# Optimization experiments

Hardware: AMD Instinct MI355X
Metric: run time of the kernel (lower is better)

Reference implementation:

```python
import jax, jax.numpy as jnp
import numpy as np

D = 128      # input_dim (= out_channels = edge_dim)
H = 2        # n_head
N_ENT = 100000
B = 64       # number of queries / batches
R = 500      # number of relations
E = 400000   # number of original edges
NEG = 0.2    # GATv2 leaky_relu negative slope


def setup_inputs() -> dict:
    key = jax.random.key(0)
    ks = jax.random.split(key, 10)
    s = 1.0 / np.sqrt(D)
    queries = jax.random.normal(ks[0], (B, D), jnp.float32)
    entities = jax.random.normal(ks[1], (N_ENT, D), jnp.float32)
    edge_index = jax.random.randint(ks[2], (2, E), 0, N_ENT)
    relations = jax.random.normal(ks[3], (R, D), jnp.float32)
    relation_index = jax.random.randint(ks[4], (E,), 0, R)
    # guarantees batch.max()+1 == queries.shape[0] (module assert)
    batch = jnp.arange(N_ENT, dtype=jnp.int32) % B
    # GATv2Conv params: lin_l / lin_r (bias=True), lin_edge (bias=False), att, bias
    W_l = jax.random.normal(ks[5], (H * D, D), jnp.float32) * s
    b_l = jnp.zeros((H * D,), jnp.float32)
    W_r = jax.random.normal(ks[6], (H * D, D), jnp.float32) * s
    b_r = jnp.zeros((H * D,), jnp.float32)
    W_ea = jax.random.normal(ks[7], (H * D, D), jnp.float32) * s
    att = jax.random.normal(ks[8], (H, D), jnp.float32) * s
    bias = jnp.zeros((D,), jnp.float32)  # concat=False -> size out_channels
    # outer Injector.lin_edge: Linear(H*D, D, bias=True)
    W_le = jax.random.normal(ks[9], (D, H * D), jnp.float32) / np.sqrt(H * D)
    b_le = jnp.zeros((D,), jnp.float32)
    return dict(queries=queries, entities=entities, edge_index=edge_index,
                relations=relations, relation_index=relation_index, batch=batch,
                W_l=W_l, b_l=b_l, W_r=W_r, b_r=b_r, W_ea=W_ea, att=att,
                bias=bias, W_le=W_le, b_le=b_le)


def reference(queries, entities, edge_index, relations, relation_index, batch,
              W_l, b_l, W_r, b_r, W_ea, att, bias, W_le, b_le):
    n_ent = entities.shape[0]
    node = jnp.vstack([entities, queries])                        # [N+B, D]
    rel_feat = jnp.vstack([relations,
                           jnp.ones((1, relations.shape[1]), relations.dtype)])
    # added edges: query -> its entities
    src = jnp.concatenate([edge_index[0], batch.astype(edge_index.dtype) + n_ent])
    tgt = jnp.concatenate([edge_index[1],
                           jnp.arange(n_ent, dtype=edge_index.dtype)])
    rel_idx = jnp.concatenate([relation_index,
                               jnp.full((n_ent,), rel_feat.shape[0] - 1,
                                        relation_index.dtype)])
    edge_attr = rel_feat[rel_idx]                                  # [Etot, D]

    n_tot = node.shape[0]
    x_l = (node @ W_l.T + b_l).reshape(n_tot, H, D)                # source proj
    x_r = (node @ W_r.T + b_r).reshape(n_tot, H, D)                # target proj
    e = (edge_attr @ W_ea.T).reshape(-1, H, D)                     # [Etot, H, D]

    xj = x_l[src]                                                  # gather per edge
    z = jax.nn.leaky_relu(xj + x_r[tgt] + e, NEG)                  # [Etot, H, D]
    alpha = jnp.einsum('ehd,hd->eh', z, att)                       # [Etot, H]
    # segment softmax over target nodes
    amax = jax.ops.segment_max(alpha, tgt, num_segments=n_tot)
    alpha = jnp.exp(alpha - amax[tgt])
    denom = jax.ops.segment_sum(alpha, tgt, num_segments=n_tot)
    alpha = alpha / (denom[tgt] + 1e-16)

    msg = xj * alpha[..., None]                                    # [Etot, H, D]
    agg = jax.ops.segment_sum(msg, tgt, num_segments=n_tot)        # [Ntot, H, D]
    out = agg.mean(axis=1) + bias                                  # concat=False
    out_node = out[:n_ent]

    out_edge = jax.nn.relu(relations @ W_ea.T)                     # [R, H*D]
    out_edge = out_edge @ W_le.T + b_le                            # [R, D]
    return (out_node, out_edge)
```

## Files before the change

kernel.cpp:

```cpp
#include <hip/hip_runtime.h>
#include <math.h>

#define D 128
#define HD 256
#define N_ENT 100000
#define NBATCH 64
#define NTOT (N_ENT + NBATCH)
#define RCOUNT 500
#define E_BASE 400000
#define ETOT (E_BASE + N_ENT)
#define NEG 0.2f
#define SCAN_NB 391
#define CPAD (SCAN_NB * 256)

#define WCAST_NB 64
#define REL_NB (RCOUNT + 1)
#define PREP_NB (WCAST_NB + REL_NB)

#define GEMM_NB ((NTOT + 63) / 64)
#define HIST_NB ((ETOT + 255) / 256)
#define EDGE_NB 6250

typedef __attribute__((ext_vector_type(8))) short bf16x8;
typedef __attribute__((ext_vector_type(8))) unsigned short u16x8;
typedef __attribute__((ext_vector_type(4))) float f32x4;
typedef __attribute__((ext_vector_type(2))) float f32x2;

static __device__ __forceinline__ unsigned cvt_pk_bf16(float lo, float hi) {
  unsigned r;
  asm("v_cvt_pk_bf16_f32 %0, %1, %2" : "=v"(r) : "v"(lo), "v"(hi));
  return r;
}
static __device__ __forceinline__ unsigned short f2bf_hw(float f) {
  unsigned r;
  asm("v_cvt_pk_bf16_f32 %0, %1, %1" : "=v"(r) : "v"(f));
  return (unsigned short)r;
}
static __device__ __forceinline__ f32x2 bfpair(unsigned u) {
  f32x2 r;
  r[0] = __builtin_bit_cast(float, u << 16);
  r[1] = __builtin_bit_cast(float, u & 0xffff0000u);
  return r;
}

static __device__ __forceinline__ void lds_barrier() {
  __builtin_amdgcn_sched_barrier(0);
  asm volatile("s_waitcnt lgkmcnt(0)" ::: "memory");
  __builtin_amdgcn_sched_barrier(0);
  __builtin_amdgcn_s_barrier();
  __builtin_amdgcn_sched_barrier(0);
}

static __device__ __forceinline__ float dpp_red16(float p) {
  int t;
  t = __builtin_amdgcn_update_dpp(0, __builtin_bit_cast(int, p), 0xB1, 0xF, 0xF, true);
  p += __builtin_bit_cast(float, t);
  t = __builtin_amdgcn_update_dpp(0, __builtin_bit_cast(int, p), 0x4E, 0xF, 0xF, true);
  p += __builtin_bit_cast(float, t);
  t = __builtin_amdgcn_update_dpp(0, __builtin_bit_cast(int, p), 0x141, 0xF, 0xF, true);
  p += __builtin_bit_cast(float, t);
  t = __builtin_amdgcn_update_dpp(0, __builtin_bit_cast(int, p), 0x140, 0xF, 0xF, true);
  p += __builtin_bit_cast(float, t);
  return p;
}

__global__ __launch_bounds__(256) void k_prep(
    const float* __restrict__ W_l, const float* __restrict__ W_r,
    unsigned short* __restrict__ Wbf,
    const float* __restrict__ relations, const float* __restrict__ W_ea,
    const float* __restrict__ W_le, const float* __restrict__ b_le,
    unsigned short* __restrict__ e_rel, float* __restrict__ out_edge) {
  __shared__ float relu_p[HD];
  int bx = blockIdx.x;
  int tid = threadIdx.x;
  if (bx < WCAST_NB) {
    int e4 = (bx * 256 + tid) * 4;
    int v = e4 >> 7;
    int k = e4 & 127;
    const float* src = (v < HD) ? (W_l + (size_t)v * D + k) : (W_r + (size_t)(v - HD) * D + k);
    float4 a = *(const float4*)src;
    uint2 p;
    p.x = cvt_pk_bf16(a.x, a.y);
    p.y = cvt_pk_bf16(a.z, a.w);
    *(uint2*)(Wbf + (size_t)v * D + k) = p;
    return;
  }
  int r = bx - WCAST_NB;
  int j = tid;
  const float* w = W_ea + (size_t)j * D;
  float acc = 0.f;
  if (r < RCOUNT) {
    const float* rel = relations + (size_t)r * D;
    for (int k = 0; k < D; k += 4) {
      float4 a = *(const float4*)(rel + k);
      float4 b = *(const float4*)(w + k);
      acc += a.x * b.x + a.y * b.y + a.z * b.z + a.w * b.w;
    }
  } else {
    for (int k = 0; k < D; k += 4) {
      float4 b = *(const float4*)(w + k);
      acc += b.x + b.y + b.z + b.w;
    }
  }
  e_rel[(size_t)r * HD + j] = f2bf_hw(acc);
  if (r < RCOUNT) {
    relu_p[j] = acc > 0.f ? acc : 0.f;
    __syncthreads();
    if (j < D) {
      const float* wl = W_le + (size_t)j * HD;
      float o = b_le[j];
      for (int k = 0; k < HD; k += 4) {
        float4 p4 = *(const float4*)(relu_p + k);
        float4 w4 = *(const float4*)(wl + k);
        o += p4.x * w4.x + p4.y * w4.y + p4.z * w4.z + p4.w * w4.w;
      }
      out_edge[(size_t)r * D + j] = o;
    }
  }
}

#define LDA 136

__global__ __launch_bounds__(256) void k_gemm_mfma(
    const float* __restrict__ entities, const float* __restrict__ queries,
    const unsigned short* __restrict__ Wbf,
    const float* __restrict__ b_l, const float* __restrict__ b_r,
    unsigned short* __restrict__ x_l, unsigned short* __restrict__ x_r,
    const int* __restrict__ edge_index, const int* __restrict__ relation_index,
    const int* __restrict__ batch, int* __restrict__ counts,
    unsigned* __restrict__ tr, unsigned* __restrict__ key) {
  __shared__ unsigned short AsCs[64 * LDA];
  int tid = threadIdx.x;
  if (blockIdx.x >= GEMM_NB) {
    int e = (blockIdx.x - GEMM_NB) * 256 + tid;
    if (e < ETOT) {
      int s, t, r;
      if (e < E_BASE) {
        s = edge_index[e];
        t = edge_index[E_BASE + e];
        r = relation_index[e];
      } else {
        int i = e - E_BASE;
        s = N_ENT + batch[i];
        t = i;
        r = RCOUNT;
      }
      int rk = atomicAdd(counts + t, 1);
      tr[e] = (unsigned)t | ((unsigned)rk << 17);
      key[e] = (unsigned)s | ((unsigned)r << 17);
    }
    return;
  }
  int rb = blockIdx.x;

  {
    int rr = tid >> 2;
    int part = (tid & 3) * 32;
    int row = rb * 64 + rr;
    const float* sp;
    if (row < N_ENT) sp = entities + (size_t)row * D;
    else if (row < NTOT) sp = queries + (size_t)(row - N_ENT) * D;
    else sp = entities;
#pragma unroll
    for (int k = 0; k < 32; k += 8) {
      float4 a0 = *(const float4*)(sp + part + k);
      float4 a1 = *(const float4*)(sp + part + k + 4);
      uint4 p;
      p.x = cvt_pk_bf16(a0.x, a0.y);
      p.y = cvt_pk_bf16(a0.z, a0.w);
      p.z = cvt_pk_bf16(a1.x, a1.y);
      p.w = cvt_pk_bf16(a1.z, a1.w);
      *(uint4*)(&AsCs[rr * LDA + part + k]) = p;
    }
  }
  __syncthreads();

  int w = tid >> 6, lane = tid & 63;
  int wr = w >> 1, wc = w & 1;
  int m = lane & 15, q8 = (lane >> 4) * 8;

  bf16x8 afr[4][2];
#pragma unroll
  for (int k4 = 0; k4 < 4; k4++)
#pragma unroll
    for (int i = 0; i < 2; i++)
      afr[k4][i] = *(const bf16x8*)(&AsCs[(wr * 32 + i * 16 + m) * LDA + k4 * 32 + q8]);

  for (int ccv = 0; ccv < 4; ccv++) {
    bool isL = ccv < 2;
    const float* bv = isL ? b_l : b_r;
    unsigned short* xdst = isL ? x_l : x_r;
    int cbase = (ccv & 1) * 128;

    f32x4 acc[2][4];
#pragma unroll
    for (int i = 0; i < 2; i++)
#pragma unroll
      for (int j = 0; j < 4; j++) acc[i][j] = (f32x4){0.f, 0.f, 0.f, 0.f};

    const unsigned short* wbase = Wbf + (size_t)(ccv * 128 + wc * 64 + m) * D;
#pragma unroll
    for (int k4 = 0; k4 < 4; k4++) {
      bf16x8 bfr[4];
#pragma unroll
      for (int j = 0; j < 4; j++)
        bfr[j] = *(const bf16x8*)(wbase + (size_t)j * 16 * D + k4 * 32 + q8);
#pragma unroll
      for (int i = 0; i < 2; i++)
#pragma unroll
        for (int j = 0; j < 4; j++)
          acc[i][j] = __builtin_amdgcn_mfma_f32_16x16x32_bf16(afr[k4][i], bfr[j], acc[i][j], 0, 0, 0);
    }

    lds_barrier();
#pragma unroll
    for (int j = 0; j < 4; j++) {
      int col = wc * 64 + j * 16 + m;
      float bb = bv[cbase + col];
#pragma unroll
      for (int i = 0; i < 2; i++) {
        int row0 = wr * 32 + i * 16 + (lane >> 4) * 4;
#pragma unroll
        for (int r = 0; r < 4; r++)
          AsCs[(row0 + r) * LDA + col] = f2bf_hw(acc[i][j][r] + bb);
      }
    }
    lds_barrier();
#pragma unroll
    for (int it = 0; it < 4; it++) {
      int g = it * 256 + tid;
      int row = g >> 4, c8 = (g & 15) * 8;
      int grow = rb * 64 + row;
      if (grow < NTOT) {
        u16x8 v = *(const u16x8*)(&AsCs[row * LDA + c8]);
        *(u16x8*)(xdst + (size_t)grow * HD + cbase + c8) = v;
      }
    }
  }
}

__global__ __launch_bounds__(256) void k_scan_a(const int* __restrict__ counts, int* __restrict__ bsum) {
  __shared__ int sd[256];
  int tid = threadIdx.x;
  sd[tid] = counts[blockIdx.x * 256 + tid];
  __syncthreads();
  for (int off = 128; off > 0; off >>= 1) {
    if (tid < off) sd[tid] += sd[tid + off];
    __syncthreads();
  }
  if (tid == 0) bsum[blockIdx.x] = sd[0];
}

__global__ __launch_bounds__(256) void k_scan_b(
    const int* __restrict__ counts, const int* __restrict__ bsum,
    int* __restrict__ offsets) {
  __shared__ int s[256];
  int b = blockIdx.x, tid = threadIdx.x;
  int part = 0;
  if (tid < b) part += bsum[tid];
  if (tid + 256 < b) part += bsum[tid + 256];
  s[tid] = part;
  __syncthreads();
  for (int off = 128; off > 0; off >>= 1) {
    if (tid < off) s[tid] += s[tid + off];
    __syncthreads();
  }
  int pre_sum = s[0];
  __syncthreads();
  int v = counts[b * 256 + tid];
  s[tid] = v;
  __syncthreads();
  for (int off = 1; off < 256; off <<= 1) {
    int y = (tid >= off) ? s[tid - off] : 0;
    __syncthreads();
    s[tid] += y;
    __syncthreads();
  }
  int excl = pre_sum + s[tid] - v;
  int i = b * 256 + tid;
  if (i <= N_ENT) offsets[i] = excl;
}

__global__ void k_scatter(const unsigned* __restrict__ tr, const unsigned* __restrict__ key,
                          const int* __restrict__ offsets, unsigned* __restrict__ sorted) {
  int e = blockIdx.x * 256 + threadIdx.x;
  if (e >= ETOT) return;
  unsigned a = tr[e];
  sorted[offsets[a & 0x1FFFFu] + (a >> 17)] = key[e];
}

static __device__ __forceinline__ float edge_accum(
    u16x8 xl8, u16x8 er8, const f32x2* __restrict__ xr2,
    const f32x2* __restrict__ at2, f32x2* __restrict__ x2) {
  uint4 xu = __builtin_bit_cast(uint4, xl8);
  uint4 eu = __builtin_bit_cast(uint4, er8);
  unsigned xw[4] = {xu.x, xu.y, xu.z, xu.w};
  unsigned ew[4] = {eu.x, eu.y, eu.z, eu.w};
  f32x2 p2 = (f32x2){0.f, 0.f};
#pragma unroll
  for (int i = 0; i < 4; ++i) {
    f32x2 x = bfpair(xw[i]);
    x2[i] = x;
    f32x2 z = (x + xr2[i]) + bfpair(ew[i]);
    f32x2 zn = z * NEG;
    z[0] = fmaxf(z[0], zn[0]);
    z[1] = fmaxf(z[1], zn[1]);
    p2 += z * at2[i];
  }
  return p2[0] + p2[1];
}

__global__ __launch_bounds__(256) void k_edge(
    const unsigned short* __restrict__ x_l, const unsigned short* __restrict__ x_r,
    const unsigned short* __restrict__ e_rel, const int* __restrict__ offsets,
    const unsigned* __restrict__ sorted, const float* __restrict__ att,
    const float* __restrict__ bias, float* __restrict__ out) {
  int wv = threadIdx.x >> 6;
  int lane = threadIdx.x & 63;
  int half = lane >> 5;
  int sl = lane & 31;
  int elem = sl * 8;
  int t0 = (blockIdx.x * 4 + wv) * 4;

  const char* xlb = (const char*)x_l + elem * 2;
  const char* erb = (const char*)e_rel + elem * 2;

  f32x2 at2[4];
  {
    float4 a0 = *(const float4*)(att + elem);
    float4 a1 = *(const float4*)(att + elem + 4);
    at2[0] = (f32x2){a0.x, a0.y};
    at2[1] = (f32x2){a0.z, a0.w};
    at2[2] = (f32x2){a1.x, a1.y};
    at2[3] = (f32x2){a1.z, a1.w};
  }
  int4 ofs = *(const int4*)(offsets + t0);
  int eb[5];
  eb[0] = ofs.x; eb[1] = ofs.y; eb[2] = ofs.z; eb[3] = ofs.w;
  eb[4] = offsets[t0 + 4];

  u16x8 xr8 = __builtin_nontemporal_load((const u16x8*)(x_r + (size_t)t0 * HD + elem));

#pragma unroll
  for (int ti = 0; ti < 4; ++ti) {
    f32x2 xr2[4];
    {
      uint4 u = __builtin_bit_cast(uint4, xr8);
      xr2[0] = bfpair(u.x); xr2[1] = bfpair(u.y);
      xr2[2] = bfpair(u.z); xr2[3] = bfpair(u.w);
    }
    xr8 = __builtin_nontemporal_load((const u16x8*)(x_r + (size_t)(t0 + ti + 1) * HD + elem));

    int e0 = eb[ti], e1 = eb[ti + 1];
    f32x2 acc2[4];
    acc2[0] = acc2[1] = acc2[2] = acc2[3] = (f32x2){0.f, 0.f};
    float denom = 0.f;
    int e = e0;
    for (; e + 4 <= e1; e += 4) {
      unsigned srA = sorted[e + half];
      unsigned srB = sorted[e + 2 + half];
      u16x8 xlA = *(const u16x8*)(xlb + ((size_t)(srA & 0x1FFFFu) << 9));
      u16x8 erA = *(const u16x8*)(erb + ((size_t)(srA >> 17) << 9));
      u16x8 xlB = *(const u16x8*)(xlb + ((size_t)(srB & 0x1FFFFu) << 9));
      u16x8 erB = *(const u16x8*)(erb + ((size_t)(srB >> 17) << 9));
      f32x2 xa2[4], xb2[4];
      float pa = edge_accum(xlA, erA, xr2, at2, xa2);
      float pb = edge_accum(xlB, erB, xr2, at2, xb2);
      pa = dpp_red16(pa);
      pb = dpp_red16(pb);
      float wa = __expf(pa);
      float wb = __expf(pb);
      denom += wa + wb;
#pragma unroll
      for (int i = 0; i < 4; ++i) {
        acc2[i] += xa2[i] * wa;
        acc2[i] += xb2[i] * wb;
      }
    }
    for (; e < e1; e += 2) {
      int ee = e + half;
      bool valid = ee < e1;
      unsigned sr = sorted[valid ? ee : e0];
      u16x8 xl8 = *(const u16x8*)(xlb + ((size_t)(sr & 0x1FFFFu) << 9));
      u16x8 er8 = *(const u16x8*)(erb + ((size_t)(sr >> 17) << 9));
      f32x2 x2[4];
      float p = edge_accum(xl8, er8, xr2, at2, x2);
      p = dpp_red16(p);
      float wgt = valid ? __expf(p) : 0.f;
      denom += wgt;
#pragma unroll
      for (int i = 0; i < 4; ++i) acc2[i] += x2[i] * wgt;
    }
    denom += __shfl_xor(denom, 32, 64);
#pragma unroll
    for (int i = 0; i < 4; ++i) {
      acc2[i][0] += __shfl_xor(acc2[i][0], 32, 64);
      acc2[i][1] += __shfl_xor(acc2[i][1], 32, 64);
    }
    float inv = 0.5f / (denom + 1e-16f);
    float o[8];
#pragma unroll
    for (int i = 0; i < 4; ++i) {
      o[2 * i] = acc2[i][0] * inv;
      o[2 * i + 1] = acc2[i][1] * inv;
    }
#pragma unroll
    for (int i = 0; i < 8; ++i) o[i] += __shfl_xor(o[i], 16, 64);
    if (lane < 16) {
      int t = t0 + ti;
      int d = sl * 8;
      float4 b0 = *(const float4*)(bias + d);
      float4 b1 = *(const float4*)(bias + d + 4);
      f32x4 s0 = (f32x4){o[0] + b0.x, o[1] + b0.y, o[2] + b0.z, o[3] + b0.w};
      f32x4 s1 = (f32x4){o[4] + b1.x, o[5] + b1.y, o[6] + b1.z, o[7] + b1.w};
      __builtin_nontemporal_store(s0, (f32x4*)(out + (size_t)t * D + d));
      __builtin_nontemporal_store(s1, (f32x4*)(out + (size_t)t * D + d + 4));
    }
  }
}

extern "C" void kernel_launch(void* const* d_in, const int* in_sizes, int n_in,
                              void* d_out, int out_size, void* d_ws, size_t ws_size,
                              hipStream_t stream) {
  const float* queries = (const float*)d_in[0];
  const float* entities = (const float*)d_in[1];
  const int* edge_index = (const int*)d_in[2];
  const float* relations = (const float*)d_in[3];
  const int* relation_index = (const int*)d_in[4];
  const int* batch = (const int*)d_in[5];
  const float* W_l = (const float*)d_in[6];
  const float* b_l = (const float*)d_in[7];
  const float* W_r = (const float*)d_in[8];
  const float* b_r = (const float*)d_in[9];
  const float* W_ea = (const float*)d_in[10];
  const float* att = (const float*)d_in[11];
  const float* bias = (const float*)d_in[12];
  const float* W_le = (const float*)d_in[13];
  const float* b_le = (const float*)d_in[14];

  float* out_node = (float*)d_out;
  float* out_edge = out_node + (size_t)N_ENT * D;

  char* base = (char*)d_ws;
  size_t off = 0;
  auto take = [&](size_t nbytes) -> void* {
    void* p = base + off;
    off += (nbytes + 255) & ~(size_t)255;
    return p;
  };
  unsigned short* x_l = (unsigned short*)take((size_t)NTOT * HD * sizeof(unsigned short));
  unsigned short* x_r = (unsigned short*)take((size_t)NTOT * HD * sizeof(unsigned short));
  unsigned short* e_rel = (unsigned short*)take((size_t)(RCOUNT + 1) * HD * sizeof(unsigned short));
  unsigned short* Wbf = (unsigned short*)take((size_t)512 * D * sizeof(unsigned short));
  int* counts = (int*)take((size_t)CPAD * sizeof(int));
  int* offsets = (int*)take((size_t)(N_ENT + 1) * sizeof(int));
  unsigned* tr = (unsigned*)take((size_t)ETOT * sizeof(unsigned));
  unsigned* key = (unsigned*)take((size_t)ETOT * sizeof(unsigned));
  int* bsum = (int*)take(512 * sizeof(int));
  unsigned* sorted = (unsigned*)take((size_t)ETOT * sizeof(unsigned));

  hipMemsetAsync(counts, 0, (size_t)CPAD * sizeof(int), stream);
  k_prep<<<dim3(PREP_NB), dim3(256), 0, stream>>>(W_l, W_r, Wbf, relations, W_ea, W_le, b_le,
                                                  e_rel, out_edge);
  k_gemm_mfma<<<dim3(GEMM_NB + HIST_NB), dim3(256), 0, stream>>>(entities, queries, Wbf, b_l, b_r,
                                                                 x_l, x_r, edge_index, relation_index,
                                                                 batch, counts, tr, key);
  k_scan_a<<<dim3(SCAN_NB), dim3(256), 0, stream>>>(counts, bsum);
  k_scan_b<<<dim3(SCAN_NB), dim3(256), 0, stream>>>(counts, bsum, offsets);
  k_scatter<<<dim3(HIST_NB), dim3(256), 0, stream>>>(tr, key, offsets, sorted);
  k_edge<<<dim3(EDGE_NB), dim3(256), 0, stream>>>(x_l, x_r, e_rel, offsets, sorted, att, bias, out_node);
}
```

Before: 285.9 us.

## Fold relation prep into GEMM launch and compute block sums via atomics

Moves the relation projection and out_edge computation from the prep kernel into extra blocks of the GEMM/histogram kernel, leaving prep to only cast weights. The histogram blocks now also atomically accumulate per-256-node block sums, which removes the separate scan_a reduction kernel. The bsum array is placed after counts so one memset clears both. This cuts two launches and a pass over counts, at the cost of an extra global atomic per edge on a small, heavily contended array.

Result: slower. 509.0 us (+78.0%).

```diff
diff --git a/kernel.cpp b/kernel.cpp
--- a/kernel.cpp
+++ b/kernel.cpp
@@ -15,7 +15,6 @@
 
 #define WCAST_NB 64
 #define REL_NB (RCOUNT + 1)
-#define PREP_NB (WCAST_NB + REL_NB)
 
 #define GEMM_NB ((NTOT + 63) / 64)
 #define HIST_NB ((ETOT + 255) / 256)
@@ -66,57 +65,16 @@
 
 __global__ __launch_bounds__(256) void k_prep(
     const float* __restrict__ W_l, const float* __restrict__ W_r,
-    unsigned short* __restrict__ Wbf,
-    const float* __restrict__ relations, const float* __restrict__ W_ea,
-    const float* __restrict__ W_le, const float* __restrict__ b_le,
-    unsigned short* __restrict__ e_rel, float* __restrict__ out_edge) {
-  __shared__ float relu_p[HD];
-  int bx = blockIdx.x;
-  int tid = threadIdx.x;
-  if (bx < WCAST_NB) {
-    int e4 = (bx * 256 + tid) * 4;
-    int v = e4 >> 7;
-    int k = e4 & 127;
-    const float* src = (v < HD) ? (W_l + (size_t)v * D + k) : (W_r + (size_t)(v - HD) * D + k);
-    float4 a = *(const float4*)src;
-    uint2 p;
-    p.x = cvt_pk_bf16(a.x, a.y);
-    p.y = cvt_pk_bf16(a.z, a.w);
-    *(uint2*)(Wbf + (size_t)v * D + k) = p;
-    return;
-  }
-  int r = bx - WCAST_NB;
-  int j = tid;
-  const float* w = W_ea + (size_t)j * D;
-  float acc = 0.f;
-  if (r < RCOUNT) {
-    const float* rel = relations + (size_t)r * D;
-    for (int k = 0; k < D; k += 4) {
-      float4 a = *(const float4*)(rel + k);
-      float4 b = *(const float4*)(w + k);
-      acc += a.x * b.x + a.y * b.y + a.z * b.z + a.w * b.w;
-    }
-  } else {
-    for (int k = 0; k < D; k += 4) {
-      float4 b = *(const float4*)(w + k);
-      acc += b.x + b.y + b.z + b.w;
-    }
-  }
-  e_rel[(size_t)r * HD + j] = f2bf_hw(acc);
-  if (r < RCOUNT) {
-    relu_p[j] = acc > 0.f ? acc : 0.f;
-    __syncthreads();
-    if (j < D) {
-      const float* wl = W_le + (size_t)j * HD;
-      float o = b_le[j];
-      for (int k = 0; k < HD; k += 4) {
-        float4 p4 = *(const float4*)(relu_p + k);
-        float4 w4 = *(const float4*)(wl + k);
-        o += p4.x * w4.x + p4.y * w4.y + p4.z * w4.z + p4.w * w4.w;
-      }
-      out_edge[(size_t)r * D + j] = o;
-    }
-  }
+    unsigned short* __restrict__ Wbf) {
+  int e4 = (blockIdx.x * 256 + threadIdx.x) * 4;
+  int v = e4 >> 7;
+  int k = e4 & 127;
+  const float* src = (v < HD) ? (W_l + (size_t)v * D + k) : (W_r + (size_t)(v - HD) * D + k);
+  float4 a = *(const float4*)src;
+  uint2 p;
+  p.x = cvt_pk_bf16(a.x, a.y);
+  p.y = cvt_pk_bf16(a.z, a.w);
+  *(uint2*)(Wbf + (size_t)v * D + k) = p;
 }
 
 #define LDA 136
@@ -127,10 +85,49 @@
     const float* __restrict__ b_l, const float* __restrict__ b_r,
     unsigned short* __restrict__ x_l, unsigned short* __restrict__ x_r,
     const int* __restrict__ edge_index, const int* __restrict__ relation_index,
-    const int* __restrict__ batch, int* __restrict__ counts,
-    unsigned* __restrict__ tr, unsigned* __restrict__ key) {
+    const int* __restrict__ batch, int* __restrict__ counts, int* __restrict__ bsum,
+    unsigned* __restrict__ tr, unsigned* __restrict__ key,
+    const float* __restrict__ relations, const float* __restrict__ W_ea,
+    const float* __restrict__ W_le, const float* __restrict__ b_le,
+    unsigned short* __restrict__ e_rel, float* __restrict__ out_edge) {
   __shared__ unsigned short AsCs[64 * LDA];
   int tid = threadIdx.x;
+  if (blockIdx.x >= GEMM_NB + HIST_NB) {
+    float* relu_p = (float*)AsCs;
+    int r = blockIdx.x - (GEMM_NB + HIST_NB);
+    int j = tid;
+    const float* w = W_ea + (size_t)j * D;
+    float acc = 0.f;
+    if (r < RCOUNT) {
+      const float* rel = relations + (size_t)r * D;
+      for (int k = 0; k < D; k += 4) {
+        float4 a = *(const float4*)(rel + k);
+        float4 b = *(const float4*)(w + k);
+        acc += a.x * b.x + a.y * b.y + a.z * b.z + a.w * b.w;
+      }
+    } else {
+      for (int k = 0; k < D; k += 4) {
+        float4 b = *(const float4*)(w + k);
+        acc += b.x + b.y + b.z + b.w;
+      }
+    }
+    e_rel[(size_t)r * HD + j] = f2bf_hw(acc);
+    if (r < RCOUNT) {
+      relu_p[j] = acc > 0.f ? acc : 0.f;
+      __syncthreads();
+      if (j < D) {
+        const float* wl = W_le + (size_t)j * HD;
+        float o = b_le[j];
+        for (int k = 0; k < HD; k += 4) {
+          float4 p4 = *(const float4*)(relu_p + k);
+          float4 w4 = *(const float4*)(wl + k);
+          o += p4.x * w4.x + p4.y * w4.y + p4.z * w4.z + p4.w * w4.w;
+        }
+        out_edge[(size_t)r * D + j] = o;
+      }
+    }
+    return;
+  }
   if (blockIdx.x >= GEMM_NB) {
     int e = (blockIdx.x - GEMM_NB) * 256 + tid;
     if (e < ETOT) {
@@ -146,6 +143,7 @@
         r = RCOUNT;
       }
       int rk = atomicAdd(counts + t, 1);
+      atomicAdd(bsum + (t >> 8), 1);
       tr[e] = (unsigned)t | ((unsigned)rk << 17);
       key[e] = (unsigned)s | ((unsigned)r << 17);
     }
@@ -239,19 +237,7 @@
   }
 }
 
-__global__ __launch_bounds__(256) void k_scan_a(const int* __restrict__ counts, int* __restrict__ bsum) {
-  __shared__ int sd[256];
-  int tid = threadIdx.x;
-  sd[tid] = counts[blockIdx.x * 256 + tid];
-  __syncthreads();
-  for (int off = 128; off > 0; off >>= 1) {
-    if (tid < off) sd[tid] += sd[tid + off];
-    __syncthreads();
-  }
-  if (tid == 0) bsum[blockIdx.x] = sd[0];
-}
-
-__global__ __launch_bounds__(256) void k_scan_b(
+__global__ __launch_bounds__(256) void k_scan(
     const int* __restrict__ counts, const int* __restrict__ bsum,
     int* __restrict__ offsets) {
   __shared__ int s[256];
@@ -452,21 +438,19 @@
   unsigned short* x_r = (unsigned short*)take((size_t)NTOT * HD * sizeof(unsigned short));
   unsigned short* e_rel = (unsigned short*)take((size_t)(RCOUNT + 1) * HD * sizeof(unsigned short));
   unsigned short* Wbf = (unsigned short*)take((size_t)512 * D * sizeof(unsigned short));
-  int* counts = (int*)take((size_t)CPAD * sizeof(int));
+  int* counts = (int*)take((size_t)(CPAD + 512) * sizeof(int));
+  int* bsum = counts + CPAD;
   int* offsets = (int*)take((size_t)(N_ENT + 1) * sizeof(int));
   unsigned* tr = (unsigned*)take((size_t)ETOT * sizeof(unsigned));
   unsigned* key = (unsigned*)take((size_t)ETOT * sizeof(unsigned));
-  int* bsum = (int*)take(512 * sizeof(int));
   unsigned* sorted = (unsigned*)take((size_t)ETOT * sizeof(unsigned));
 
-  hipMemsetAsync(counts, 0, (size_t)CPAD * sizeof(int), stream);
-  k_prep<<<dim3(PREP_NB), dim3(256), 0, stream>>>(W_l, W_r, Wbf, relations, W_ea, W_le, b_le,
-                                                  e_rel, out_edge);
-  k_gemm_mfma<<<dim3(GEMM_NB + HIST_NB), dim3(256), 0, stream>>>(entities, queries, Wbf, b_l, b_r,
-                                                                 x_l, x_r, edge_index, relation_index,
-                                                                 batch, counts, tr, key);
-  k_scan_a<<<dim3(SCAN_NB), dim3(256), 0, stream>>>(counts, bsum);
-  k_scan_b<<<dim3(SCAN_NB), dim3(256), 0, stream>>>(counts, bsum, offsets);
+  hipMemsetAsync(counts, 0, (size_t)(CPAD + 512) * sizeof(int), stream);
+  k_prep<<<dim3(WCAST_NB), dim3(256), 0, stream>>>(W_l, W_r, Wbf);
+  k_gemm_mfma<<<dim3(GEMM_NB + HIST_NB + REL_NB), dim3(256), 0, stream>>>(
+      entities, queries, Wbf, b_l, b_r, x_l, x_r, edge_index, relation_index, batch,
+      counts, bsum, tr, key, relations, W_ea, W_le, b_le, e_rel, out_edge);
+  k_scan<<<dim3(SCAN_NB), dim3(256), 0, stream>>>(counts, bsum, offsets);
   k_scatter<<<dim3(HIST_NB), dim3(256), 0, stream>>>(tr, key, offsets, sorted);
   k_edge<<<dim3(EDGE_NB), dim3(256), 0, stream>>>(x_l, x_r, e_rel, offsets, sorted, att, bias, out_node);
 }
```
